# Optimization experiments

Hardware: AMD Instinct MI355X
Metric: run time of the kernel (lower is better)

The kernel has to match this reference:

```python
import jax, jax.numpy as jnp
import numpy as np

D = 1024
H = 16
DH = D // H  # 64
SCALE = DH ** (-0.5)

def setup_inputs() -> dict:
    key = jax.random.key(0)
    k1, k2, k3, k4, k5 = jax.random.split(key, 5)
    x = jax.random.normal(k1, (4, 2048, D), dtype=jnp.float32)
    w_qkv = jax.random.normal(k2, (D, 3 * D), dtype=jnp.float32) * (D ** -0.5)
    b_qkv = jax.random.normal(k3, (3 * D,), dtype=jnp.float32) * 0.02
    w_out = jax.random.normal(k4, (D, D), dtype=jnp.float32) * (D ** -0.5)
    b_out = jax.random.normal(k5, (D,), dtype=jnp.float32) * 0.02
    return {"x": x, "w_qkv": w_qkv, "b_qkv": b_qkv, "w_out": w_out, "b_out": b_out}

def reference(x, w_qkv, b_qkv, w_out, b_out):
    B, S, C = x.shape
    qkv = x @ w_qkv + b_qkv                          # [B,S,3D]
    qkv = qkv.reshape(B, S, 3, H, DH)
    qkv = jnp.transpose(qkv, (0, 3, 2, 1, 4))        # [B,H,3,S,DH]
    q, k, v = qkv[:, :, 0], qkv[:, :, 1], qkv[:, :, 2]
    q = q * SCALE
    scores = jnp.einsum('bhqd,bhkd->bhqk', q, k)     # [B,H,S,S]
    attn = jax.nn.softmax(scores.astype(jnp.float32), axis=-1).astype(scores.dtype)
    out = jnp.einsum('bhqk,bhkd->bhqd', attn, v)     # [B,H,S,DH]
    out = jnp.transpose(out, (0, 2, 1, 3)).reshape(B, S, C)
    return out @ w_out + b_out
```

## Files before the change

### kernel.cpp

```cpp
#include <hip/hip_runtime.h>

#define D_ 1024
#define H_ 16
#define DH_ 64
#define S_ 2048
#define B_ 4
#define N_ (B_*S_)
#define M3_ 3072
#define QSC_ 0.18033688011112042f

typedef _Float16 f16;
typedef _Float16 f16x8 __attribute__((ext_vector_type(8)));
typedef _Float16 f16x4 __attribute__((ext_vector_type(4)));
typedef _Float16 f16x2 __attribute__((ext_vector_type(2)));
typedef __fp16   h16x2 __attribute__((ext_vector_type(2)));
typedef float    f32x4 __attribute__((ext_vector_type(4)));

typedef __attribute__((address_space(1))) void gvoid;
typedef __attribute__((address_space(3))) void lvoid;

__device__ __forceinline__ void gl16(const f16* g, f16* l) {
    __builtin_amdgcn_global_load_lds((gvoid*)g, (lvoid*)l, 16, 0, 0);
}

__device__ __forceinline__ f16x2 pk_cvt(float a, float b) {
#if __has_builtin(__builtin_amdgcn_cvt_pkrtz)
    h16x2 t = __builtin_amdgcn_cvt_pkrtz(a, b);
    return __builtin_bit_cast(f16x2, t);
#else
    f16x2 r; r[0] = (f16)a; r[1] = (f16)b; return r;
#endif
}

__global__ __launch_bounds__(256) void cvt_x_kernel(const float* __restrict__ in,
                                                    f16* __restrict__ out) {
    size_t i = ((size_t)blockIdx.x * 256 + threadIdx.x) * 4;
    float4 f = *reinterpret_cast<const float4*>(in + i);
    f16x4 o;
    o[0] = (f16)f.x; o[1] = (f16)f.y; o[2] = (f16)f.z; o[3] = (f16)f.w;
    *reinterpret_cast<f16x4*>(out + i) = o;
}

__global__ __launch_bounds__(256) void wt_cvt_kernel(const float* __restrict__ in,
                                                     f16* __restrict__ out,
                                                     int K, int Nc) {
    __shared__ float tile[32][33];
    int tx = threadIdx.x & 31, ty = threadIdx.x >> 5;
    int c = blockIdx.x * 32 + tx;
    #pragma unroll
    for (int i = 0; i < 4; i++) {
        int r = blockIdx.y * 32 + ty + i * 8;
        tile[ty + i * 8][tx] = in[(size_t)r * Nc + c];
    }
    __syncthreads();
    #pragma unroll
    for (int i = 0; i < 4; i++) {
        int r2 = blockIdx.x * 32 + ty + i * 8;
        int c2 = blockIdx.y * 32 + tx;
        out[(size_t)r2 * K + c2] = (f16)tile[tx][ty + i * 8];
    }
}

__global__ __launch_bounds__(256) void gemm_qkv_kernel(
        const f16* __restrict__ A, const f16* __restrict__ Bt,
        const float* __restrict__ bias,
        f16* __restrict__ qo, f16* __restrict__ ko, f16* __restrict__ vTo) {
    __shared__ __align__(16) f16 As[128 * 32];
    __shared__ __align__(16) f16 Bs[128 * 32];
    const int tid  = threadIdx.x;
    const int lane = tid & 63, w = tid >> 6;
    const int quad = lane >> 4, lrow = lane & 15;
    const int wm = (w & 1) * 64, wn = (w >> 1) * 64;
    const int n0 = blockIdx.x * 128, m0 = blockIdx.y * 128;

    f32x4 acc[4][4];
    #pragma unroll
    for (int i = 0; i < 4; i++)
        #pragma unroll
        for (int j = 0; j < 4; j++) acc[i][j] = {0.f, 0.f, 0.f, 0.f};

    const int ar0 = tid >> 2, ap0 = tid & 3;
    const f16* Ag0 = A  + (size_t)(n0 + ar0) * D_ + ap0 * 8;
    const f16* Ag1 = Ag0 + (size_t)64 * D_;
    const f16* Bg0 = Bt + (size_t)(m0 + ar0) * D_ + ap0 * 8;
    const f16* Bg1 = Bg0 + (size_t)64 * D_;
    f16* Asl = As + tid * 8;
    f16* Bsl = Bs + tid * 8;

    for (int kt = 0; kt < D_ / 32; kt++) {
        gl16(Ag0 + kt * 32, Asl);
        gl16(Ag1 + kt * 32, Asl + 64 * 32);
        gl16(Bg0 + kt * 32, Bsl);
        gl16(Bg1 + kt * 32, Bsl + 64 * 32);
        __syncthreads();
        f16x8 af[4], bf[4];
        #pragma unroll
        for (int i = 0; i < 4; i++)
            af[i] = *reinterpret_cast<const f16x8*>(&As[(wm + i * 16 + lrow) * 32 + quad * 8]);
        #pragma unroll
        for (int j = 0; j < 4; j++)
            bf[j] = *reinterpret_cast<const f16x8*>(&Bs[(wn + j * 16 + lrow) * 32 + quad * 8]);
        #pragma unroll
        for (int i = 0; i < 4; i++)
            #pragma unroll
            for (int j = 0; j < 4; j++)
                acc[i][j] = __builtin_amdgcn_mfma_f32_16x16x32_f16(af[i], bf[j], acc[i][j], 0, 0, 0);
        __syncthreads();
    }

    #pragma unroll
    for (int j = 0; j < 4; j++) {
        int m   = m0 + wn + j * 16 + lrow;
        int sec = m >> 10;
        int hd  = m & 1023;
        int hh  = hd >> 6, d = hd & 63;
        float bb = bias[m];
        if (sec == 2) {
            #pragma unroll
            for (int i = 0; i < 4; i++) {
                int n = n0 + wm + i * 16 + quad * 4;
                int bidx = n >> 11, s = n & 2047;
                f16x4 o;
                #pragma unroll
                for (int r = 0; r < 4; r++) o[r] = (f16)(acc[i][j][r] + bb);
                *reinterpret_cast<f16x4*>(
                    &vTo[(((size_t)(bidx * H_ + hh)) * DH_ + d) * S_ + s]) = o;
            }
        } else {
            f16* dst = (sec == 0) ? qo : ko;
            float sc = (sec == 0) ? QSC_ : 1.0f;
            #pragma unroll
            for (int i = 0; i < 4; i++) {
                #pragma unroll
                for (int r = 0; r < 4; r++) {
                    int n = n0 + wm + i * 16 + quad * 4 + r;
                    int bidx = n >> 11, s = n & 2047;
                    dst[(((size_t)(bidx * H_ + hh)) * S_ + s) * DH_ + d] =
                        (f16)((acc[i][j][r] + bb) * sc);
                }
            }
        }
    }
}

__global__ __launch_bounds__(256) void attn_kernel(
        const f16* __restrict__ q, const f16* __restrict__ k,
        const f16* __restrict__ vT, f16* __restrict__ ctx) {
    __shared__ __align__(16) f16 Ks[2][128 * 72];
    __shared__ __align__(16) f16 Vs[2][64 * 136];
    const int tid  = threadIdx.x;
    const int lane = tid & 63, w = tid >> 6;
    const int quad = lane >> 4, lrow = lane & 15;
    const int id = blockIdx.x;
    const int bh = id & 63;
    const int q0 = (id >> 6) * 256;
    const int b  = bh >> 4, h = bh & 15;
    const f16* qb = q  + (size_t)bh * S_ * DH_;
    const f16* kb = k  + (size_t)bh * S_ * DH_;
    const f16* vb = vT + (size_t)bh * DH_ * S_;

    f16x8 qf[4][2];
    #pragma unroll
    for (int f = 0; f < 4; f++)
        #pragma unroll
        for (int hf = 0; hf < 2; hf++)
            qf[f][hf] = *reinterpret_cast<const f16x8*>(
                qb + (size_t)(q0 + w * 64 + f * 16 + lrow) * DH_ + hf * 32 + quad * 8);

    f16x8 ones8;
    #pragma unroll
    for (int i = 0; i < 8; i++) ones8[i] = (f16)1.f;

    f32x4 lacc[4];
    f32x4 ot[4][4];
    #pragma unroll
    for (int f = 0; f < 4; f++) {
        lacc[f] = {0.f, 0.f, 0.f, 0.f};
        #pragma unroll
        for (int dj = 0; dj < 4; dj++) ot[f][dj] = {0.f, 0.f, 0.f, 0.f};
    }

    int kslot[4], kpart[4], vrow[4], vpart[4];
    #pragma unroll
    for (int i = 0; i < 4; i++) {
        int ch = tid + i * 256;
        int g = ch >> 3, jj = g & 7, qd = (g >> 3) & 3;
        kslot[i] = (g & ~31) + ((jj >> 2) << 4) + (qd << 2) + (jj & 3);
        kpart[i] = ch & 7;
        vrow[i] = ch >> 4; vpart[i] = ch & 15;
    }

    f16x8 krg[4], vrg[4];
    #pragma unroll
    for (int i = 0; i < 4; i++) {
        int ch = tid + i * 256;
        krg[i] = *reinterpret_cast<const f16x8*>(kb + (size_t)(ch >> 3) * DH_ + (ch & 7) * 8);
        vrg[i] = *reinterpret_cast<const f16x8*>(vb + (size_t)vrow[i] * S_ + vpart[i] * 8);
    }
    #pragma unroll
    for (int i = 0; i < 4; i++) {
        *reinterpret_cast<f16x8*>(&Ks[0][kslot[i] * 72 + kpart[i] * 8]) = krg[i];
        *reinterpret_cast<f16x8*>(&Vs[0][vrow[i] * 136 + vpart[i] * 8]) = vrg[i];
    }
    #pragma unroll
    for (int i = 0; i < 4; i++) {
        int ch = tid + i * 256;
        krg[i] = *reinterpret_cast<const f16x8*>(kb + (size_t)(128 + (ch >> 3)) * DH_ + (ch & 7) * 8);
        vrg[i] = *reinterpret_cast<const f16x8*>(vb + (size_t)vrow[i] * S_ + 128 + vpart[i] * 8);
    }
    __syncthreads();

    const int NT = S_ / 128;
    for (int kt = 0; kt < NT; kt++) {
        const int cur = kt & 1;
        const f16* Kc = Ks[cur];
        const f16* Vc = Vs[cur];

        #pragma unroll
        for (int t = 0; t < 4; t++) {
            f16x8 p8[4];
            #pragma unroll
            for (int half = 0; half < 2; half++) {
                int mb = 2 * t + half;
                f16x8 kf0 = *reinterpret_cast<const f16x8*>(&Kc[(mb * 16 + lrow) * 72 + quad * 8]);
                f16x8 kf1 = *reinterpret_cast<const f16x8*>(&Kc[(mb * 16 + lrow) * 72 + 32 + quad * 8]);
                #pragma unroll
                for (int f = 0; f < 4; f++) {
                    f32x4 st = {0.f, 0.f, 0.f, 0.f};
                    st = __builtin_amdgcn_mfma_f32_16x16x32_f16(kf0, qf[f][0], st, 0, 0, 0);
                    st = __builtin_amdgcn_mfma_f32_16x16x32_f16(kf1, qf[f][1], st, 0, 0, 0);
                    f16x2 lo = pk_cvt(__builtin_amdgcn_exp2f(st[0]),
                                      __builtin_amdgcn_exp2f(st[1]));
                    f16x2 hi = pk_cvt(__builtin_amdgcn_exp2f(st[2]),
                                      __builtin_amdgcn_exp2f(st[3]));
                    p8[f][half * 4 + 0] = lo[0]; p8[f][half * 4 + 1] = lo[1];
                    p8[f][half * 4 + 2] = hi[0]; p8[f][half * 4 + 3] = hi[1];
                }
            }
            #pragma unroll
            for (int dj = 0; dj < 4; dj++) {
                f16x8 vf = *reinterpret_cast<const f16x8*>(
                    &Vc[(dj * 16 + lrow) * 136 + t * 32 + quad * 8]);
                #pragma unroll
                for (int f = 0; f < 4; f++)
                    ot[f][dj] = __builtin_amdgcn_mfma_f32_16x16x32_f16(vf, p8[f], ot[f][dj], 0, 0, 0);
            }
            #pragma unroll
            for (int f = 0; f < 4; f++)
                lacc[f] = __builtin_amdgcn_mfma_f32_16x16x32_f16(ones8, p8[f], lacc[f], 0, 0, 0);
        }

        if (kt + 1 < NT) {
            const int nxt = cur ^ 1;
            #pragma unroll
            for (int i = 0; i < 4; i++) {
                *reinterpret_cast<f16x8*>(&Ks[nxt][kslot[i] * 72 + kpart[i] * 8]) = krg[i];
                *reinterpret_cast<f16x8*>(&Vs[nxt][vrow[i] * 136 + vpart[i] * 8]) = vrg[i];
            }
            if (kt + 2 < NT) {
                const int kv2 = (kt + 2) * 128;
                #pragma unroll
                for (int i = 0; i < 4; i++) {
                    int ch = tid + i * 256;
                    krg[i] = *reinterpret_cast<const f16x8*>(kb + (size_t)(kv2 + (ch >> 3)) * DH_ + (ch & 7) * 8);
                    vrg[i] = *reinterpret_cast<const f16x8*>(vb + (size_t)vrow[i] * S_ + kv2 + vpart[i] * 8);
                }
            }
            __syncthreads();
        }
    }

    #pragma unroll
    for (int f = 0; f < 4; f++) {
        float inv = 1.0f / lacc[f][0];
        int qrow = q0 + w * 64 + f * 16 + lrow;
        #pragma unroll
        for (int dj = 0; dj < 4; dj++) {
            f16x4 o;
            #pragma unroll
            for (int r = 0; r < 4; r++) o[r] = (f16)(ot[f][dj][r] * inv);
            *reinterpret_cast<f16x4*>(
                &ctx[((size_t)(b * S_ + qrow)) * D_ + h * DH_ + dj * 16 + quad * 4]) = o;
        }
    }
}

__global__ __launch_bounds__(256) void gemm_out_kernel(
        const f16* __restrict__ A, const f16* __restrict__ Bt,
        const float* __restrict__ bias, float* __restrict__ out) {
    __shared__ __align__(16) f16 As[128 * 32];
    __shared__ __align__(16) f16 Bs[128 * 32];
    const int tid  = threadIdx.x;
    const int lane = tid & 63, w = tid >> 6;
    const int quad = lane >> 4, lrow = lane & 15;
    const int wm = (w & 1) * 64, wn = (w >> 1) * 64;
    const int n0 = blockIdx.x * 128, m0 = blockIdx.y * 128;

    f32x4 acc[4][4];
    #pragma unroll
    for (int i = 0; i < 4; i++)
        #pragma unroll
        for (int j = 0; j < 4; j++) acc[i][j] = {0.f, 0.f, 0.f, 0.f};

    const int ar0 = tid >> 2, ap0 = tid & 3;
    const f16* Ag0 = A  + (size_t)(n0 + ar0) * D_ + ap0 * 8;
    const f16* Ag1 = Ag0 + (size_t)64 * D_;
    const f16* Bg0 = Bt + (size_t)(m0 + ar0) * D_ + ap0 * 8;
    const f16* Bg1 = Bg0 + (size_t)64 * D_;
    f16* Asl = As + tid * 8;
    f16* Bsl = Bs + tid * 8;

    for (int kt = 0; kt < D_ / 32; kt++) {
        gl16(Ag0 + kt * 32, Asl);
        gl16(Ag1 + kt * 32, Asl + 64 * 32);
        gl16(Bg0 + kt * 32, Bsl);
        gl16(Bg1 + kt * 32, Bsl + 64 * 32);
        __syncthreads();
        f16x8 af[4], bf[4];
        #pragma unroll
        for (int i = 0; i < 4; i++)
            af[i] = *reinterpret_cast<const f16x8*>(&As[(wm + i * 16 + lrow) * 32 + quad * 8]);
        #pragma unroll
        for (int j = 0; j < 4; j++)
            bf[j] = *reinterpret_cast<const f16x8*>(&Bs[(wn + j * 16 + lrow) * 32 + quad * 8]);
        #pragma unroll
        for (int i = 0; i < 4; i++)
            #pragma unroll
            for (int j = 0; j < 4; j++)
                acc[i][j] = __builtin_amdgcn_mfma_f32_16x16x32_f16(af[i], bf[j], acc[i][j], 0, 0, 0);
        __syncthreads();
    }

    #pragma unroll
    for (int j = 0; j < 4; j++) {
        int m = m0 + wn + j * 16 + lrow;
        float bb = bias[m];
        #pragma unroll
        for (int i = 0; i < 4; i++)
            #pragma unroll
            for (int r = 0; r < 4; r++) {
                int n = n0 + wm + i * 16 + quad * 4 + r;
                out[(size_t)n * D_ + m] = acc[i][j][r] + bb;
            }
    }
}

extern "C" void kernel_launch(void* const* d_in, const int* in_sizes, int n_in,
                              void* d_out, int out_size, void* d_ws, size_t ws_size,
                              hipStream_t stream) {
    (void)in_sizes; (void)n_in; (void)out_size; (void)ws_size;
    const float* x     = (const float*)d_in[0];
    const float* w_qkv = (const float*)d_in[1];
    const float* b_qkv = (const float*)d_in[2];
    const float* w_out = (const float*)d_in[3];
    const float* b_out = (const float*)d_in[4];
    float* out = (float*)d_out;

    char* ws = (char*)d_ws;
    const size_t MB = 1024 * 1024;
    f16* xb    = (f16*)(ws);
    f16* wqkvT = (f16*)(ws + 16 * MB);
    f16* woutT = (f16*)(ws + 22 * MB);
    f16* qs    = (f16*)(ws + 24 * MB);
    f16* kk    = (f16*)(ws + 40 * MB);
    f16* vTb   = (f16*)(ws + 72 * MB);
    f16* ctx   = xb;

    cvt_x_kernel<<<(N_ * D_) / (256 * 4), 256, 0, stream>>>(x, xb);
    wt_cvt_kernel<<<dim3(M3_ / 32, D_ / 32), 256, 0, stream>>>(w_qkv, wqkvT, D_, M3_);
    wt_cvt_kernel<<<dim3(D_ / 32, D_ / 32), 256, 0, stream>>>(w_out, woutT, D_, D_);
    gemm_qkv_kernel<<<dim3(N_ / 128, M3_ / 128), 256, 0, stream>>>(xb, wqkvT, b_qkv, qs, kk, vTb);
    attn_kernel<<<(B_ * H_) * (S_ / 256), 256, 0, stream>>>(qs, kk, vTb, ctx);
    gemm_out_kernel<<<dim3(N_ / 128, D_ / 128), 256, 0, stream>>>(ctx, woutT, b_out, out);
}
```

Before: 270.8 us.

## Double GEMM K-tile to 64 and single-buffer attention K/V shared memory

The QKV and output projection GEMMs now stage a 64-wide K slice per iteration instead of 32, which halves the number of barrier pairs and load rounds per tile. The shared buffers double in size, and the unpadded 64-element row stride may cause LDS bank conflicts on fragment reads. The attention kernel drops its double-buffered K/V LDS tiles for a single buffer, prefetching the next tile into registers while computing, with two barriers per iteration. This halves the attention kernel's LDS footprint so more blocks can be resident, at the cost of an extra sync per tile.

```diff
diff --git a/kernel.cpp b/kernel.cpp
--- a/kernel.cpp
+++ b/kernel.cpp
@@ -65,8 +65,8 @@
         const f16* __restrict__ A, const f16* __restrict__ Bt,
         const float* __restrict__ bias,
         f16* __restrict__ qo, f16* __restrict__ ko, f16* __restrict__ vTo) {
-    __shared__ __align__(16) f16 As[128 * 32];
-    __shared__ __align__(16) f16 Bs[128 * 32];
+    __shared__ __align__(16) f16 As[128 * 64];
+    __shared__ __align__(16) f16 Bs[128 * 64];
     const int tid  = threadIdx.x;
     const int lane = tid & 63, w = tid >> 6;
     const int quad = lane >> 4, lrow = lane & 15;
@@ -79,32 +79,34 @@
         #pragma unroll
         for (int j = 0; j < 4; j++) acc[i][j] = {0.f, 0.f, 0.f, 0.f};
 
-    const int ar0 = tid >> 2, ap0 = tid & 3;
-    const f16* Ag0 = A  + (size_t)(n0 + ar0) * D_ + ap0 * 8;
-    const f16* Ag1 = Ag0 + (size_t)64 * D_;
-    const f16* Bg0 = Bt + (size_t)(m0 + ar0) * D_ + ap0 * 8;
-    const f16* Bg1 = Bg0 + (size_t)64 * D_;
+    const int srow = tid >> 3, spart = tid & 7;
+    const f16* Ag = A  + (size_t)(n0 + srow) * D_ + spart * 8;
+    const f16* Bg = Bt + (size_t)(m0 + srow) * D_ + spart * 8;
     f16* Asl = As + tid * 8;
     f16* Bsl = Bs + tid * 8;
 
-    for (int kt = 0; kt < D_ / 32; kt++) {
-        gl16(Ag0 + kt * 32, Asl);
-        gl16(Ag1 + kt * 32, Asl + 64 * 32);
-        gl16(Bg0 + kt * 32, Bsl);
-        gl16(Bg1 + kt * 32, Bsl + 64 * 32);
-        __syncthreads();
-        f16x8 af[4], bf[4];
-        #pragma unroll
-        for (int i = 0; i < 4; i++)
-            af[i] = *reinterpret_cast<const f16x8*>(&As[(wm + i * 16 + lrow) * 32 + quad * 8]);
-        #pragma unroll
-        for (int j = 0; j < 4; j++)
-            bf[j] = *reinterpret_cast<const f16x8*>(&Bs[(wn + j * 16 + lrow) * 32 + quad * 8]);
-        #pragma unroll
-        for (int i = 0; i < 4; i++)
+    for (int kt = 0; kt < D_ / 64; kt++) {
+        #pragma unroll
+        for (int i = 0; i < 4; i++) {
+            gl16(Ag + (size_t)(i * 32) * D_ + kt * 64, Asl + i * 2048);
+            gl16(Bg + (size_t)(i * 32) * D_ + kt * 64, Bsl + i * 2048);
+        }
+        __syncthreads();
+        #pragma unroll
+        for (int s = 0; s < 2; s++) {
+            f16x8 af[4], bf[4];
+            #pragma unroll
+            for (int i = 0; i < 4; i++)
+                af[i] = *reinterpret_cast<const f16x8*>(&As[(wm + i * 16 + lrow) * 64 + s * 32 + quad * 8]);
             #pragma unroll
             for (int j = 0; j < 4; j++)
-                acc[i][j] = __builtin_amdgcn_mfma_f32_16x16x32_f16(af[i], bf[j], acc[i][j], 0, 0, 0);
+                bf[j] = *reinterpret_cast<const f16x8*>(&Bs[(wn + j * 16 + lrow) * 64 + s * 32 + quad * 8]);
+            #pragma unroll
+            for (int i = 0; i < 4; i++)
+                #pragma unroll
+                for (int j = 0; j < 4; j++)
+                    acc[i][j] = __builtin_amdgcn_mfma_f32_16x16x32_f16(af[i], bf[j], acc[i][j], 0, 0, 0);
+        }
         __syncthreads();
     }
 
@@ -146,8 +148,8 @@
 __global__ __launch_bounds__(256) void attn_kernel(
         const f16* __restrict__ q, const f16* __restrict__ k,
         const f16* __restrict__ vT, f16* __restrict__ ctx) {
-    __shared__ __align__(16) f16 Ks[2][128 * 72];
-    __shared__ __align__(16) f16 Vs[2][64 * 136];
+    __shared__ __align__(16) f16 Ks[128 * 72];
+    __shared__ __align__(16) f16 Vs[64 * 136];
     const int tid  = threadIdx.x;
     const int lane = tid & 63, w = tid >> 6;
     const int quad = lane >> 4, lrow = lane & 15;
@@ -197,24 +199,24 @@
         krg[i] = *reinterpret_cast<const f16x8*>(kb + (size_t)(ch >> 3) * DH_ + (ch & 7) * 8);
         vrg[i] = *reinterpret_cast<const f16x8*>(vb + (size_t)vrow[i] * S_ + vpart[i] * 8);
     }
-    #pragma unroll
-    for (int i = 0; i < 4; i++) {
-        *reinterpret_cast<f16x8*>(&Ks[0][kslot[i] * 72 + kpart[i] * 8]) = krg[i];
-        *reinterpret_cast<f16x8*>(&Vs[0][vrow[i] * 136 + vpart[i] * 8]) = vrg[i];
-    }
-    #pragma unroll
-    for (int i = 0; i < 4; i++) {
-        int ch = tid + i * 256;
-        krg[i] = *reinterpret_cast<const f16x8*>(kb + (size_t)(128 + (ch >> 3)) * DH_ + (ch & 7) * 8);
-        vrg[i] = *reinterpret_cast<const f16x8*>(vb + (size_t)vrow[i] * S_ + 128 + vpart[i] * 8);
-    }
-    __syncthreads();
 
     const int NT = S_ / 128;
     for (int kt = 0; kt < NT; kt++) {
-        const int cur = kt & 1;
-        const f16* Kc = Ks[cur];
-        const f16* Vc = Vs[cur];
+        #pragma unroll
+        for (int i = 0; i < 4; i++) {
+            *reinterpret_cast<f16x8*>(&Ks[kslot[i] * 72 + kpart[i] * 8]) = krg[i];
+            *reinterpret_cast<f16x8*>(&Vs[vrow[i] * 136 + vpart[i] * 8]) = vrg[i];
+        }
+        __syncthreads();
+        if (kt + 1 < NT) {
+            const int kv1 = (kt + 1) * 128;
+            #pragma unroll
+            for (int i = 0; i < 4; i++) {
+                int ch = tid + i * 256;
+                krg[i] = *reinterpret_cast<const f16x8*>(kb + (size_t)(kv1 + (ch >> 3)) * DH_ + (ch & 7) * 8);
+                vrg[i] = *reinterpret_cast<const f16x8*>(vb + (size_t)vrow[i] * S_ + kv1 + vpart[i] * 8);
+            }
+        }
 
         #pragma unroll
         for (int t = 0; t < 4; t++) {
@@ -222,8 +224,8 @@
             #pragma unroll
             for (int half = 0; half < 2; half++) {
                 int mb = 2 * t + half;
-                f16x8 kf0 = *reinterpret_cast<const f16x8*>(&Kc[(mb * 16 + lrow) * 72 + quad * 8]);
-                f16x8 kf1 = *reinterpret_cast<const f16x8*>(&Kc[(mb * 16 + lrow) * 72 + 32 + quad * 8]);
+                f16x8 kf0 = *reinterpret_cast<const f16x8*>(&Ks[(mb * 16 + lrow) * 72 + quad * 8]);
+                f16x8 kf1 = *reinterpret_cast<const f16x8*>(&Ks[(mb * 16 + lrow) * 72 + 32 + quad * 8]);
                 #pragma unroll
                 for (int f = 0; f < 4; f++) {
                     f32x4 st = {0.f, 0.f, 0.f, 0.f};
@@ -240,7 +242,7 @@
             #pragma unroll
             for (int dj = 0; dj < 4; dj++) {
                 f16x8 vf = *reinterpret_cast<const f16x8*>(
-                    &Vc[(dj * 16 + lrow) * 136 + t * 32 + quad * 8]);
+                    &Vs[(dj * 16 + lrow) * 136 + t * 32 + quad * 8]);
                 #pragma unroll
                 for (int f = 0; f < 4; f++)
                     ot[f][dj] = __builtin_amdgcn_mfma_f32_16x16x32_f16(vf, p8[f], ot[f][dj], 0, 0, 0);
@@ -249,25 +251,7 @@
             for (int f = 0; f < 4; f++)
                 lacc[f] = __builtin_amdgcn_mfma_f32_16x16x32_f16(ones8, p8[f], lacc[f], 0, 0, 0);
         }
-
-        if (kt + 1 < NT) {
-            const int nxt = cur ^ 1;
-            #pragma unroll
-            for (int i = 0; i < 4; i++) {
-                *reinterpret_cast<f16x8*>(&Ks[nxt][kslot[i] * 72 + kpart[i] * 8]) = krg[i];
-                *reinterpret_cast<f16x8*>(&Vs[nxt][vrow[i] * 136 + vpart[i] * 8]) = vrg[i];
-            }
-            if (kt + 2 < NT) {
-                const int kv2 = (kt + 2) * 128;
-                #pragma unroll
-                for (int i = 0; i < 4; i++) {
-                    int ch = tid + i * 256;
-                    krg[i] = *reinterpret_cast<const f16x8*>(kb + (size_t)(kv2 + (ch >> 3)) * DH_ + (ch & 7) * 8);
-                    vrg[i] = *reinterpret_cast<const f16x8*>(vb + (size_t)vrow[i] * S_ + kv2 + vpart[i] * 8);
-                }
-            }
-            __syncthreads();
-        }
+        __syncthreads();
     }
 
     #pragma unroll
@@ -288,8 +272,8 @@
 __global__ __launch_bounds__(256) void gemm_out_kernel(
         const f16* __restrict__ A, const f16* __restrict__ Bt,
         const float* __restrict__ bias, float* __restrict__ out) {
-    __shared__ __align__(16) f16 As[128 * 32];
-    __shared__ __align__(16) f16 Bs[128 * 32];
+    __shared__ __align__(16) f16 As[128 * 64];
+    __shared__ __align__(16) f16 Bs[128 * 64];
     const int tid  = threadIdx.x;
     const int lane = tid & 63, w = tid >> 6;
     const int quad = lane >> 4, lrow = lane & 15;
@@ -302,32 +286,34 @@
         #pragma unroll
         for (int j = 0; j < 4; j++) acc[i][j] = {0.f, 0.f, 0.f, 0.f};
 
-    const int ar0 = tid >> 2, ap0 = tid & 3;
-    const f16* Ag0 = A  + (size_t)(n0 + ar0) * D_ + ap0 * 8;
-    const f16* Ag1 = Ag0 + (size_t)64 * D_;
-    const f16* Bg0 = Bt + (size_t)(m0 + ar0) * D_ + ap0 * 8;
-    const f16* Bg1 = Bg0 + (size_t)64 * D_;
+    const int srow = tid >> 3, spart = tid & 7;
+    const f16* Ag = A  + (size_t)(n0 + srow) * D_ + spart * 8;
+    const f16* Bg = Bt + (size_t)(m0 + srow) * D_ + spart * 8;
     f16* Asl = As + tid * 8;
     f16* Bsl = Bs + tid * 8;
 
-    for (int kt = 0; kt < D_ / 32; kt++) {
-        gl16(Ag0 + kt * 32, Asl);
-        gl16(Ag1 + kt * 32, Asl + 64 * 32);
-        gl16(Bg0 + kt * 32, Bsl);
-        gl16(Bg1 + kt * 32, Bsl + 64 * 32);
-        __syncthreads();
-        f16x8 af[4], bf[4];
-        #pragma unroll
-        for (int i = 0; i < 4; i++)
-            af[i] = *reinterpret_cast<const f16x8*>(&As[(wm + i * 16 + lrow) * 32 + quad * 8]);
-        #pragma unroll
-        for (int j = 0; j < 4; j++)
-            bf[j] = *reinterpret_cast<const f16x8*>(&Bs[(wn + j * 16 + lrow) * 32 + quad * 8]);
-        #pragma unroll
-        for (int i = 0; i < 4; i++)
+    for (int kt = 0; kt < D_ / 64; kt++) {
+        #pragma unroll
+        for (int i = 0; i < 4; i++) {
+            gl16(Ag + (size_t)(i * 32) * D_ + kt * 64, Asl + i * 2048);
+            gl16(Bg + (size_t)(i * 32) * D_ + kt * 64, Bsl + i * 2048);
+        }
+        __syncthreads();
+        #pragma unroll
+        for (int s = 0; s < 2; s++) {
+            f16x8 af[4], bf[4];
+            #pragma unroll
+            for (int i = 0; i < 4; i++)
+                af[i] = *reinterpret_cast<const f16x8*>(&As[(wm + i * 16 + lrow) * 64 + s * 32 + quad * 8]);
             #pragma unroll
             for (int j = 0; j < 4; j++)
-                acc[i][j] = __builtin_amdgcn_mfma_f32_16x16x32_f16(af[i], bf[j], acc[i][j], 0, 0, 0);
+                bf[j] = *reinterpret_cast<const f16x8*>(&Bs[(wn + j * 16 + lrow) * 64 + s * 32 + quad * 8]);
+            #pragma unroll
+            for (int i = 0; i < 4; i++)
+                #pragma unroll
+                for (int j = 0; j < 4; j++)
+                    acc[i][j] = __builtin_amdgcn_mfma_f32_16x16x32_f16(af[i], bf[j], acc[i][j], 0, 0, 0);
+        }
         __syncthreads();
     }
 
```

Measured after the change: 283.7 us. +4.8%, slower.
